# Performance work log

Measured on AMD Instinct MI355X. Metric: run time of the kernel, lower is better.

The kernel has to match this reference:

```python
import jax, jax.numpy as jnp
import numpy as np

IN_F, OUT_F, GROUP, KROT, PACK, BATCH = 4096, 14336, 128, 8, 8, 16


def _pack_nibbles(nib):
    # nib: int32 in [0,16) with shape [R, C]; pack 8 consecutive cols into one int32
    shifts = 4 * jnp.arange(PACK, dtype=jnp.int32)
    return jnp.sum(nib.reshape(nib.shape[0], -1, PACK) << shifts, axis=-1).astype(jnp.int32)


def setup_inputs() -> dict:
    key = jax.random.key(0)
    ks = jax.random.split(key, 7)
    n_groups = IN_F // GROUP
    x = jax.random.normal(ks[0], (BATCH, IN_F), dtype=jnp.float16)
    theta = (0.1 * jax.random.normal(ks[1], (KROT, IN_F // 2), dtype=jnp.float32)).astype(jnp.float16)
    # each rotation round pairs channels via a permutation: (pairs[k,2i], pairs[k,2i+1])
    pairs = jnp.stack([
        jax.random.permutation(jax.random.fold_in(ks[2], k), IN_F)
        for k in range(KROT)
    ]).astype(jnp.int32)
    channel_scales = (1.0 + 0.01 * jax.random.normal(ks[3], (1, IN_F), dtype=jnp.float32)).astype(jnp.float16)
    qweight = _pack_nibbles(jax.random.randint(ks[4], (IN_F, OUT_F), 0, 16, dtype=jnp.int32))
    qzeros = _pack_nibbles(jax.random.randint(ks[5], (n_groups, OUT_F), 0, 16, dtype=jnp.int32))
    scales = (0.001 + 0.01 * jax.random.uniform(ks[6], (n_groups, OUT_F), dtype=jnp.float32)).astype(jnp.float16)
    return {"x": x, "theta": theta, "pairs": pairs, "channel_scales": channel_scales,
            "qweight": qweight, "qzeros": qzeros, "scales": scales}


def _rotate(x, theta, pairs, channel_scales):
    # KROT rounds of pairwise Givens rotations, then per-channel scaling
    cos = jnp.cos(theta.astype(jnp.float32)).astype(x.dtype)  # [KROT, IN/2]
    sin = jnp.sin(theta.astype(jnp.float32)).astype(x.dtype)
    for k in range(theta.shape[0]):
        ia, ib = pairs[k, 0::2], pairs[k, 1::2]
        a, b = x[..., ia], x[..., ib]
        x = x.at[..., ia].set(cos[k] * a - sin[k] * b).at[..., ib].set(sin[k] * a + cos[k] * b)
    return x * channel_scales


def _dequant(qweight, qzeros, scales, group_size, dtype):
    shifts = 4 * jnp.arange(PACK, dtype=jnp.int32)
    iw = ((qweight[:, :, None] >> shifts) & 0xF).reshape(qweight.shape[0], -1)  # [IN, OUT]
    iz = ((qzeros[:, :, None] >> shifts) & 0xF).reshape(qzeros.shape[0], -1)    # [n_groups, OUT]
    w = (iw - jnp.repeat(iz, group_size, axis=0)).astype(dtype)
    return w * jnp.repeat(scales, group_size, axis=0)


def reference(x, theta, pairs, channel_scales, qweight, qzeros, scales):
    group_size = x.shape[-1] // qzeros.shape[0]
    xr = _rotate(x, theta, pairs, channel_scales)
    w = _dequant(qweight, qzeros, scales, group_size, xr.dtype)  # [IN, OUT] fp16
    return xr @ w  # [BATCH, OUT]
```

## Files before the change

kernel.cpp:

```cpp
#include <hip/hip_runtime.h>
#include <cstdint>

#define IN_F   4096
#define OUT_F  14336
#define GROUP  128
#define KROT   8
#define BATCH  16
#define NJP    1792
#define NG     32

typedef __attribute__((ext_vector_type(8))) short short8;
typedef __attribute__((ext_vector_type(4))) float f32x4;

__device__ uint32_t g_xa[BATCH * IN_F / 2];
__device__ float    g_rs[NG * BATCH];
__device__ float    g_part[4 * BATCH * OUT_F];

static __device__ __forceinline__ unsigned short f2bf(float f) {
    union { float f; uint32_t i; } v; v.f = f;
    uint32_t u = v.i;
    uint32_t r = u + 0x7FFFu + ((u >> 16) & 1u);
    return (unsigned short)(r >> 16);
}
static __device__ __forceinline__ float bf2f(uint32_t u16) {
    union { uint32_t i; float f; } v; v.i = u16 << 16; return v.f;
}

__global__ __launch_bounds__(1024) void k_rotate(
    const float* __restrict__ x,
    const float* __restrict__ theta,
    const int*   __restrict__ pairs,
    const float* __restrict__ cscale)
{
    __shared__ float row[IN_F];
    const int b   = blockIdx.x;
    const int tid = threadIdx.x;

    int2  ij0[KROT], ij1[KROT];
    float c0[KROT], s0[KROT], c1[KROT], s1[KROT];
#pragma unroll
    for (int k = 0; k < KROT; ++k) {
        const int2*  pk = (const int2*)(pairs + k * IN_F);
        const float* tk = theta + k * (IN_F / 2);
        ij0[k] = pk[tid];
        ij1[k] = pk[tid + 1024];
        __sincosf(tk[tid],        &s0[k], &c0[k]);
        __sincosf(tk[tid + 1024], &s1[k], &c1[k]);
    }

    for (int i = tid; i < IN_F; i += 1024) row[i] = x[b * IN_F + i];
    __syncthreads();

#pragma unroll
    for (int k = 0; k < KROT; ++k) {
        float a0 = row[ij0[k].x], b0 = row[ij0[k].y];
        float a1 = row[ij1[k].x], b1 = row[ij1[k].y];
        row[ij0[k].x] = c0[k] * a0 - s0[k] * b0;
        row[ij0[k].y] = s0[k] * a0 + c0[k] * b0;
        row[ij1[k].x] = c1[k] * a1 - s1[k] * b1;
        row[ij1[k].y] = s1[k] * a1 + c1[k] * b1;
        __syncthreads();
    }

    float p0, p1;
    {
        int i = tid;
        uint32_t lo = f2bf(row[2 * i]     * cscale[2 * i]);
        uint32_t hi = f2bf(row[2 * i + 1] * cscale[2 * i + 1]);
        g_xa[b * (IN_F / 2) + i] = lo | (hi << 16);
        p0 = bf2f(lo) + bf2f(hi);
        i = tid + 1024;
        lo = f2bf(row[2 * i]     * cscale[2 * i]);
        hi = f2bf(row[2 * i + 1] * cscale[2 * i + 1]);
        g_xa[b * (IN_F / 2) + i] = lo | (hi << 16);
        p1 = bf2f(lo) + bf2f(hi);
    }
#pragma unroll
    for (int m = 1; m < 64; m <<= 1) {
        p0 += __shfl_xor(p0, m, 64);
        p1 += __shfl_xor(p1, m, 64);
    }
    if ((tid & 63) == 0) {
        const int w = tid >> 6;
        g_rs[w * BATCH + b]        = p0;
        g_rs[(16 + w) * BATCH + b] = p1;
    }
}

__global__ __launch_bounds__(256) void k_gemm(
    const int*   __restrict__ qweight,
    const int*   __restrict__ qzeros,
    const float* __restrict__ scales)
{
    __shared__ uint4 ldsb[128 * 17];

    const int tid   = threadIdx.x;
    const int bn    = blockIdx.x % 112;
    const int bk    = blockIdx.x / 112;
    const int n0    = bn * 128;
    const int jp0   = n0 >> 3;
    const int jp    = tid & 15;
    const int koct  = tid >> 4;
    const int lane  = tid & 63;
    const int wv    = tid >> 6;
    const int mrow  = lane & 15;
    const int quad  = lane >> 4;
    const int xsw   = koct ^ (jp & 7);

    const int nl0 = wv * 32 + mrow;
    const int nl1 = nl0 + 16;
    const int sw0 = (nl0 >> 3) & 7;
    const int sw1 = (nl1 >> 3) & 7;

    float s0v[8], s1v[8], zf0[8], zf1[8];
    f32x4 rsv[8];
    {
        const int jz0 = jp0 + (nl0 >> 3);
        const int jz1 = jp0 + (nl1 >> 3);
        const int sh  = 4 * (mrow & 7);
#pragma unroll
        for (int g = 0; g < 8; ++g) {
            const int gg = bk * 8 + g;
            s0v[g] = scales[(size_t)gg * OUT_F + n0 + nl0];
            s1v[g] = scales[(size_t)gg * OUT_F + n0 + nl1];
            zf0[g] = 128.0f + (float)(((uint32_t)qzeros[gg * NJP + jz0] >> sh) & 15u);
            zf1[g] = 128.0f + (float)(((uint32_t)qzeros[gg * NJP + jz1] >> sh) & 15u);
            rsv[g] = *(const f32x4*)(g_rs + gg * BATCH + quad * 4);
        }
    }

    f32x4 m0 = {0.f, 0.f, 0.f, 0.f};
    f32x4 m1 = {0.f, 0.f, 0.f, 0.f};

    for (int st = 0; st < 8; ++st) {
        const int g   = bk * 8 + st;
        const int kr0 = g * GROUP + koct * 8;

        uint32_t wc[8];
#pragma unroll
        for (int i = 0; i < 8; ++i)
            wc[i] = (uint32_t)qweight[(size_t)(kr0 + i) * NJP + jp0 + jp];

        uint4 ac[4];
        const uint32_t* apst = g_xa + mrow * (IN_F / 2) + bk * 512 + st * 64 + quad * 4;
#pragma unroll
        for (int kt = 0; kt < 4; ++kt) ac[kt] = *(const uint4*)(apst + kt * 16);

#pragma unroll
        for (int c = 0; c < 8; ++c) {
            uint4 cell;
            uint32_t pk[4];
#pragma unroll
            for (int h = 0; h < 4; ++h) {
                uint32_t lo = (wc[2 * h]     >> (4 * c)) & 15u;
                uint32_t hi = (wc[2 * h + 1] >> (4 * c)) & 15u;
                pk[h] = 0x43004300u | lo | (hi << 16);
            }
            cell.x = pk[0]; cell.y = pk[1]; cell.z = pk[2]; cell.w = pk[3];
            ldsb[(jp * 8 + c) * 17 + xsw] = cell;
        }
        __syncthreads();

        f32x4 ga = {0.f, 0.f, 0.f, 0.f};
        f32x4 gb = {0.f, 0.f, 0.f, 0.f};
#pragma unroll
        for (int kt = 0; kt < 4; ++kt) {
            union { uint4 q; short8 s; } af, b0, b1;
            af.q = ac[kt];
            const int ko = kt * 4 + quad;
            b0.q = ldsb[nl0 * 17 + (ko ^ sw0)];
            b1.q = ldsb[nl1 * 17 + (ko ^ sw1)];
            ga = __builtin_amdgcn_mfma_f32_16x16x32_bf16(af.s, b0.s, ga, 0, 0, 0);
            gb = __builtin_amdgcn_mfma_f32_16x16x32_bf16(af.s, b1.s, gb, 0, 0, 0);
        }

        const float t0 = s0v[st] * zf0[st];
        const float t1 = s1v[st] * zf1[st];
#pragma unroll
        for (int r = 0; r < 4; ++r) {
            m0[r] = fmaf(s0v[st], ga[r], fmaf(-t0, rsv[st][r], m0[r]));
            m1[r] = fmaf(s1v[st], gb[r], fmaf(-t1, rsv[st][r], m1[r]));
        }
        __syncthreads();
    }

    float* pp = g_part + (size_t)bk * BATCH * OUT_F;
#pragma unroll
    for (int r = 0; r < 4; ++r) {
        const int row = quad * 4 + r;
        pp[(size_t)row * OUT_F + n0 + nl0] = m0[r];
        pp[(size_t)row * OUT_F + n0 + nl1] = m1[r];
    }
}

__global__ __launch_bounds__(128) void k_reduce(float* __restrict__ out)
{
    const int t = blockIdx.x * 128 + threadIdx.x;
    const size_t j = (size_t)t * 4;
    float4 a = *(const float4*)(g_part + j);
    float4 b = *(const float4*)(g_part + (size_t)BATCH * OUT_F + j);
    float4 c = *(const float4*)(g_part + (size_t)2 * BATCH * OUT_F + j);
    float4 d = *(const float4*)(g_part + (size_t)3 * BATCH * OUT_F + j);
    float4 s;
    s.x = (a.x + b.x) + (c.x + d.x);
    s.y = (a.y + b.y) + (c.y + d.y);
    s.z = (a.z + b.z) + (c.z + d.z);
    s.w = (a.w + b.w) + (c.w + d.w);
    *(float4*)(out + j) = s;
}

extern "C" void kernel_launch(void* const* d_in, const int* in_sizes, int n_in,
                              void* d_out, int out_size, void* d_ws, size_t ws_size,
                              hipStream_t stream) {
    const float* x       = (const float*)d_in[0];
    const float* theta   = (const float*)d_in[1];
    const int*   pairs   = (const int*)d_in[2];
    const float* cscale  = (const float*)d_in[3];
    const int*   qweight = (const int*)d_in[4];
    const int*   qzeros  = (const int*)d_in[5];
    const float* scales  = (const float*)d_in[6];
    float*       out     = (float*)d_out;
    (void)d_ws; (void)ws_size;

    k_rotate<<<16, 1024, 0, stream>>>(x, theta, pairs, cscale);
    k_gemm<<<448, 256, 0, stream>>>(qweight, qzeros, scales);
    k_reduce<<<(BATCH * OUT_F) / (128 * 4), 128, 0, stream>>>(out);
}
```

Measured before the change: 107.6 us.

## Fuse split-K reduction into GEMM via per-wave K split and LDS reduce

Each block now covers 32 output columns with its four waves splitting K, and sums the partials in LDS before writing the output directly. This removes the global partial buffer, the separate reduce kernel launch, and the block-wide barriers in the K loop, since each wave uses a private LDS region. In exchange, global weight loads become narrower per row (16-byte segments), which may reduce coalescing efficiency.

```diff
diff --git a/kernel.cpp b/kernel.cpp
--- a/kernel.cpp
+++ b/kernel.cpp
@@ -14,7 +14,6 @@
 
 __device__ uint32_t g_xa[BATCH * IN_F / 2];
 __device__ float    g_rs[NG * BATCH];
-__device__ float    g_part[4 * BATCH * OUT_F];
 
 static __device__ __forceinline__ unsigned short f2bf(float f) {
     union { float f; uint32_t i; } v; v.f = f;
@@ -90,29 +89,30 @@
 __global__ __launch_bounds__(256) void k_gemm(
     const int*   __restrict__ qweight,
     const int*   __restrict__ qzeros,
-    const float* __restrict__ scales)
+    const float* __restrict__ scales,
+    float*       __restrict__ out)
 {
-    __shared__ uint4 ldsb[128 * 17];
-
-    const int tid   = threadIdx.x;
-    const int bn    = blockIdx.x % 112;
-    const int bk    = blockIdx.x / 112;
-    const int n0    = bn * 128;
-    const int jp0   = n0 >> 3;
-    const int jp    = tid & 15;
-    const int koct  = tid >> 4;
-    const int lane  = tid & 63;
-    const int wv    = tid >> 6;
-    const int mrow  = lane & 15;
-    const int quad  = lane >> 4;
-    const int xsw   = koct ^ (jp & 7);
-
-    const int nl0 = wv * 32 + mrow;
-    const int nl1 = nl0 + 16;
-    const int sw0 = (nl0 >> 3) & 7;
-    const int sw1 = (nl1 >> 3) & 7;
-
-    float s0v[8], s1v[8], zf0[8], zf1[8];
+    __shared__ uint4 ldsb[4 * 32 * 17];
+
+    const int tid  = threadIdx.x;
+    const int bn   = blockIdx.x;
+    const int n0   = bn * 32;
+    const int jp0  = bn * 4;
+    const int w    = tid >> 6;
+    const int lane = tid & 63;
+    const int jps  = lane & 3;
+    const int koct = lane >> 2;
+    const int mrow = lane & 15;
+    const int quad = lane >> 4;
+    const int nl0  = mrow;
+    const int nl1  = mrow + 16;
+    const int sw0  = mrow >> 3;
+    const int sw1  = 2 + (mrow >> 3);
+    const int xsw  = koct ^ jps;
+
+    uint4* ldsw = ldsb + w * (32 * 17);
+
+    float s0v[8], s1v[8], t0v[8], t1v[8];
     f32x4 rsv[8];
     {
         const int jz0 = jp0 + (nl0 >> 3);
@@ -120,11 +120,13 @@
         const int sh  = 4 * (mrow & 7);
 #pragma unroll
         for (int g = 0; g < 8; ++g) {
-            const int gg = bk * 8 + g;
+            const int gg = w * 8 + g;
             s0v[g] = scales[(size_t)gg * OUT_F + n0 + nl0];
             s1v[g] = scales[(size_t)gg * OUT_F + n0 + nl1];
-            zf0[g] = 128.0f + (float)(((uint32_t)qzeros[gg * NJP + jz0] >> sh) & 15u);
-            zf1[g] = 128.0f + (float)(((uint32_t)qzeros[gg * NJP + jz1] >> sh) & 15u);
+            const float z0 = 128.0f + (float)(((uint32_t)qzeros[gg * NJP + jz0] >> sh) & 15u);
+            const float z1 = 128.0f + (float)(((uint32_t)qzeros[gg * NJP + jz1] >> sh) & 15u);
+            t0v[g] = s0v[g] * z0;
+            t1v[g] = s1v[g] * z1;
             rsv[g] = *(const f32x4*)(g_rs + gg * BATCH + quad * 4);
         }
     }
@@ -133,16 +135,16 @@
     f32x4 m1 = {0.f, 0.f, 0.f, 0.f};
 
     for (int st = 0; st < 8; ++st) {
-        const int g   = bk * 8 + st;
+        const int g   = w * 8 + st;
         const int kr0 = g * GROUP + koct * 8;
 
         uint32_t wc[8];
 #pragma unroll
         for (int i = 0; i < 8; ++i)
-            wc[i] = (uint32_t)qweight[(size_t)(kr0 + i) * NJP + jp0 + jp];
+            wc[i] = (uint32_t)qweight[(size_t)(kr0 + i) * NJP + jp0 + jps];
 
         uint4 ac[4];
-        const uint32_t* apst = g_xa + mrow * (IN_F / 2) + bk * 512 + st * 64 + quad * 4;
+        const uint32_t* apst = g_xa + mrow * (IN_F / 2) + w * 512 + st * 64 + quad * 4;
 #pragma unroll
         for (int kt = 0; kt < 4; ++kt) ac[kt] = *(const uint4*)(apst + kt * 16);
 
@@ -157,9 +159,8 @@
                 pk[h] = 0x43004300u | lo | (hi << 16);
             }
             cell.x = pk[0]; cell.y = pk[1]; cell.z = pk[2]; cell.w = pk[3];
-            ldsb[(jp * 8 + c) * 17 + xsw] = cell;
-        }
-        __syncthreads();
+            ldsw[(jps * 8 + c) * 17 + xsw] = cell;
+        }
 
         f32x4 ga = {0.f, 0.f, 0.f, 0.f};
         f32x4 gb = {0.f, 0.f, 0.f, 0.f};
@@ -168,45 +169,41 @@
             union { uint4 q; short8 s; } af, b0, b1;
             af.q = ac[kt];
             const int ko = kt * 4 + quad;
-            b0.q = ldsb[nl0 * 17 + (ko ^ sw0)];
-            b1.q = ldsb[nl1 * 17 + (ko ^ sw1)];
+            b0.q = ldsw[nl0 * 17 + (ko ^ sw0)];
+            b1.q = ldsw[nl1 * 17 + (ko ^ sw1)];
             ga = __builtin_amdgcn_mfma_f32_16x16x32_bf16(af.s, b0.s, ga, 0, 0, 0);
             gb = __builtin_amdgcn_mfma_f32_16x16x32_bf16(af.s, b1.s, gb, 0, 0, 0);
         }
 
-        const float t0 = s0v[st] * zf0[st];
-        const float t1 = s1v[st] * zf1[st];
 #pragma unroll
         for (int r = 0; r < 4; ++r) {
-            m0[r] = fmaf(s0v[st], ga[r], fmaf(-t0, rsv[st][r], m0[r]));
-            m1[r] = fmaf(s1v[st], gb[r], fmaf(-t1, rsv[st][r], m1[r]));
-        }
-        __syncthreads();
-    }
-
-    float* pp = g_part + (size_t)bk * BATCH * OUT_F;
+            m0[r] = fmaf(s0v[st], ga[r], fmaf(-t0v[st], rsv[st][r], m0[r]));
+            m1[r] = fmaf(s1v[st], gb[r], fmaf(-t1v[st], rsv[st][r], m1[r]));
+        }
+    }
+
+    float* redw = (float*)(ldsb + w * (32 * 17));
 #pragma unroll
     for (int r = 0; r < 4; ++r) {
-        const int row = quad * 4 + r;
-        pp[(size_t)row * OUT_F + n0 + nl0] = m0[r];
-        pp[(size_t)row * OUT_F + n0 + nl1] = m1[r];
-    }
-}
-
-__global__ __launch_bounds__(128) void k_reduce(float* __restrict__ out)
-{
-    const int t = blockIdx.x * 128 + threadIdx.x;
-    const size_t j = (size_t)t * 4;
-    float4 a = *(const float4*)(g_part + j);
-    float4 b = *(const float4*)(g_part + (size_t)BATCH * OUT_F + j);
-    float4 c = *(const float4*)(g_part + (size_t)2 * BATCH * OUT_F + j);
-    float4 d = *(const float4*)(g_part + (size_t)3 * BATCH * OUT_F + j);
-    float4 s;
-    s.x = (a.x + b.x) + (c.x + d.x);
-    s.y = (a.y + b.y) + (c.y + d.y);
-    s.z = (a.z + b.z) + (c.z + d.z);
-    s.w = (a.w + b.w) + (c.w + d.w);
-    *(float4*)(out + j) = s;
+        redw[(quad * 4 + r) * 16 + mrow]       = m0[r];
+        redw[256 + (quad * 4 + r) * 16 + mrow] = m1[r];
+    }
+    __syncthreads();
+
+    const float* redf = (const float*)ldsb;
+    const int col  = tid & 31;
+    const int tile = col >> 4;
+    const int c16  = col & 15;
+    const int r0   = tid >> 5;
+    float sA = 0.f, sB = 0.f;
+#pragma unroll
+    for (int ww = 0; ww < 4; ++ww) {
+        const float* base = redf + ww * (32 * 17 * 4) + tile * 256 + c16;
+        sA += base[r0 * 16];
+        sB += base[(r0 + 8) * 16];
+    }
+    out[(size_t)r0 * OUT_F + n0 + col]       = sA;
+    out[(size_t)(r0 + 8) * OUT_F + n0 + col] = sB;
 }
 
 extern "C" void kernel_launch(void* const* d_in, const int* in_sizes, int n_in,
@@ -223,6 +220,5 @@
     (void)d_ws; (void)ws_size;
 
     k_rotate<<<16, 1024, 0, stream>>>(x, theta, pairs, cscale);
-    k_gemm<<<448, 256, 0, stream>>>(qweight, qzeros, scales);
-    k_reduce<<<(BATCH * OUT_F) / (128 * 4), 128, 0, stream>>>(out);
-}
+    k_gemm<<<448, 256, 0, stream>>>(qweight, qzeros, scales, out);
+}
```

Result: slower. 127.3 us (+18.3%).

## Split K across waves in gemm, removing per-stage block barriers

Applied to the files above, without the earlier changes.

Reworks the dequant GEMM so that each wave owns two quantization groups and all 128 output columns, instead of the whole block sharing each K stage. Each wave dequantizes into its own LDS region, so the two __syncthreads per stage disappear. The four waves' partial results are then reduced through LDS once at the end and written with vectorized stores. This trades more registers per thread (8 accumulators, per-group scale tables) and an extra LDS reduction for less barrier stalling and better coalesced output. Occupancy is hinted through launch_bounds(256,2).

```diff
diff --git a/kernel.cpp b/kernel.cpp
--- a/kernel.cpp
+++ b/kernel.cpp
@@ -87,110 +87,124 @@
     }
 }
 
-__global__ __launch_bounds__(256) void k_gemm(
+__global__ __launch_bounds__(256, 2) void k_gemm(
     const int*   __restrict__ qweight,
     const int*   __restrict__ qzeros,
     const float* __restrict__ scales)
 {
-    __shared__ uint4 ldsb[128 * 17];
-
-    const int tid   = threadIdx.x;
-    const int bn    = blockIdx.x % 112;
-    const int bk    = blockIdx.x / 112;
-    const int n0    = bn * 128;
-    const int jp0   = n0 >> 3;
-    const int jp    = tid & 15;
-    const int koct  = tid >> 4;
-    const int lane  = tid & 63;
-    const int wv    = tid >> 6;
-    const int mrow  = lane & 15;
-    const int quad  = lane >> 4;
-    const int xsw   = koct ^ (jp & 7);
-
-    const int nl0 = wv * 32 + mrow;
-    const int nl1 = nl0 + 16;
-    const int sw0 = (nl0 >> 3) & 7;
-    const int sw1 = (nl1 >> 3) & 7;
-
-    float s0v[8], s1v[8], zf0[8], zf1[8];
-    f32x4 rsv[8];
+    __shared__ uint4 ldsb[4 * 512];
+
+    const int tid  = threadIdx.x;
+    const int bn   = blockIdx.x % 112;
+    const int bk   = blockIdx.x / 112;
+    const int n0   = bn * 128;
+    const int jp0  = bn * 16;
+    const int w    = tid >> 6;
+    const int lane = tid & 63;
+    const int jp   = lane & 15;
+    const int rr   = lane >> 4;
+    const int mrow = lane & 15;
+    const int quad = lane >> 4;
+
+    uint4* ldsw = ldsb + w * 512;
+
+    float sv[2][8], tv[2][8];
+    f32x4 rsv[2];
     {
-        const int jz0 = jp0 + (nl0 >> 3);
-        const int jz1 = jp0 + (nl1 >> 3);
-        const int sh  = 4 * (mrow & 7);
-#pragma unroll
-        for (int g = 0; g < 8; ++g) {
-            const int gg = bk * 8 + g;
-            s0v[g] = scales[(size_t)gg * OUT_F + n0 + nl0];
-            s1v[g] = scales[(size_t)gg * OUT_F + n0 + nl1];
-            zf0[g] = 128.0f + (float)(((uint32_t)qzeros[gg * NJP + jz0] >> sh) & 15u);
-            zf1[g] = 128.0f + (float)(((uint32_t)qzeros[gg * NJP + jz1] >> sh) & 15u);
-            rsv[g] = *(const f32x4*)(g_rs + gg * BATCH + quad * 4);
+        const int sh = 4 * (mrow & 7);
+#pragma unroll
+        for (int gi = 0; gi < 2; ++gi) {
+            const int gg = bk * 8 + w * 2 + gi;
+            rsv[gi] = *(const f32x4*)(g_rs + gg * BATCH + quad * 4);
+#pragma unroll
+            for (int t = 0; t < 8; ++t) {
+                const int col = n0 + t * 16 + mrow;
+                const float s = scales[(size_t)gg * OUT_F + col];
+                const float z = 128.0f +
+                    (float)(((uint32_t)qzeros[gg * NJP + (col >> 3)] >> sh) & 15u);
+                sv[gi][t] = s;
+                tv[gi][t] = s * z;
+            }
         }
     }
 
-    f32x4 m0 = {0.f, 0.f, 0.f, 0.f};
-    f32x4 m1 = {0.f, 0.f, 0.f, 0.f};
-
-    for (int st = 0; st < 8; ++st) {
-        const int g   = bk * 8 + st;
-        const int kr0 = g * GROUP + koct * 8;
-
-        uint32_t wc[8];
-#pragma unroll
-        for (int i = 0; i < 8; ++i)
-            wc[i] = (uint32_t)qweight[(size_t)(kr0 + i) * NJP + jp0 + jp];
-
-        uint4 ac[4];
-        const uint32_t* apst = g_xa + mrow * (IN_F / 2) + bk * 512 + st * 64 + quad * 4;
-#pragma unroll
-        for (int kt = 0; kt < 4; ++kt) ac[kt] = *(const uint4*)(apst + kt * 16);
-
-#pragma unroll
-        for (int c = 0; c < 8; ++c) {
-            uint4 cell;
-            uint32_t pk[4];
-#pragma unroll
-            for (int h = 0; h < 4; ++h) {
-                uint32_t lo = (wc[2 * h]     >> (4 * c)) & 15u;
-                uint32_t hi = (wc[2 * h + 1] >> (4 * c)) & 15u;
-                pk[h] = 0x43004300u | lo | (hi << 16);
+    f32x4 m[8];
+#pragma unroll
+    for (int t = 0; t < 8; ++t) m[t] = (f32x4){0.f, 0.f, 0.f, 0.f};
+
+#pragma unroll
+    for (int gi = 0; gi < 2; ++gi) {
+        const int gg = bk * 8 + w * 2 + gi;
+
+        f32x4 ga[8];
+#pragma unroll
+        for (int t = 0; t < 8; ++t) ga[t] = (f32x4){0.f, 0.f, 0.f, 0.f};
+
+#pragma unroll
+        for (int sc = 0; sc < 4; ++sc) {
+            const int kr0 = gg * GROUP + sc * 32 + rr * 8;
+
+            uint32_t wc[8];
+#pragma unroll
+            for (int i = 0; i < 8; ++i)
+                wc[i] = (uint32_t)qweight[(size_t)(kr0 + i) * NJP + jp0 + jp];
+
+            union { uint4 q; short8 s; } af;
+            af.q = *(const uint4*)(g_xa + mrow * (IN_F / 2)
+                                   + ((gg * GROUP + sc * 32) >> 1) + quad * 4);
+
+#pragma unroll
+            for (int cc = 0; cc < 8; ++cc) {
+                const int c  = cc ^ (jp & 7);
+                const int sh = 4 * c;
+                uint4 cell;
+                uint32_t pk[4];
+#pragma unroll
+                for (int h = 0; h < 4; ++h) {
+                    uint32_t lo = (wc[2 * h]     >> sh) & 15u;
+                    uint32_t hi = (wc[2 * h + 1] >> sh) & 15u;
+                    pk[h] = 0x43004300u | lo | (hi << 16);
+                }
+                cell.x = pk[0]; cell.y = pk[1]; cell.z = pk[2]; cell.w = pk[3];
+                ldsw[rr * 128 + jp * 8 + c] = cell;
             }
-            cell.x = pk[0]; cell.y = pk[1]; cell.z = pk[2]; cell.w = pk[3];
-            ldsb[(jp * 8 + c) * 17 + xsw] = cell;
+
+#pragma unroll
+            for (int t = 0; t < 8; ++t) {
+                union { uint4 q; short8 s; } bf;
+                bf.q = ldsw[quad * 128 + t * 16 + mrow];
+                ga[t] = __builtin_amdgcn_mfma_f32_16x16x32_bf16(af.s, bf.s, ga[t], 0, 0, 0);
+            }
         }
-        __syncthreads();
-
-        f32x4 ga = {0.f, 0.f, 0.f, 0.f};
-        f32x4 gb = {0.f, 0.f, 0.f, 0.f};
-#pragma unroll
-        for (int kt = 0; kt < 4; ++kt) {
-            union { uint4 q; short8 s; } af, b0, b1;
-            af.q = ac[kt];
-            const int ko = kt * 4 + quad;
-            b0.q = ldsb[nl0 * 17 + (ko ^ sw0)];
-            b1.q = ldsb[nl1 * 17 + (ko ^ sw1)];
-            ga = __builtin_amdgcn_mfma_f32_16x16x32_bf16(af.s, b0.s, ga, 0, 0, 0);
-            gb = __builtin_amdgcn_mfma_f32_16x16x32_bf16(af.s, b1.s, gb, 0, 0, 0);
-        }
-
-        const float t0 = s0v[st] * zf0[st];
-        const float t1 = s1v[st] * zf1[st];
-#pragma unroll
-        for (int r = 0; r < 4; ++r) {
-            m0[r] = fmaf(s0v[st], ga[r], fmaf(-t0, rsv[st][r], m0[r]));
-            m1[r] = fmaf(s1v[st], gb[r], fmaf(-t1, rsv[st][r], m1[r]));
-        }
-        __syncthreads();
-    }
-
-    float* pp = g_part + (size_t)bk * BATCH * OUT_F;
-#pragma unroll
-    for (int r = 0; r < 4; ++r) {
-        const int row = quad * 4 + r;
-        pp[(size_t)row * OUT_F + n0 + nl0] = m0[r];
-        pp[(size_t)row * OUT_F + n0 + nl1] = m1[r];
-    }
+
+#pragma unroll
+        for (int t = 0; t < 8; ++t)
+#pragma unroll
+            for (int r = 0; r < 4; ++r)
+                m[t][r] = fmaf(sv[gi][t], ga[t][r],
+                               fmaf(-tv[gi][t], rsv[gi][r], m[t][r]));
+    }
+
+    float* fw = (float*)ldsb + w * 2048;
+#pragma unroll
+    for (int t = 0; t < 8; ++t)
+#pragma unroll
+        for (int r = 0; r < 4; ++r)
+            fw[(quad * 4 + r) * 128 + t * 16 + mrow] = m[t][r];
+    __syncthreads();
+
+    const float* fb   = (const float*)ldsb;
+    const int    colg = (tid & 31) * 4;
+    const int    row  = tid >> 5;
+    f32x4 sA = {0.f, 0.f, 0.f, 0.f}, sB = {0.f, 0.f, 0.f, 0.f};
+#pragma unroll
+    for (int ww = 0; ww < 4; ++ww) {
+        sA += *(const f32x4*)(fb + ww * 2048 + row * 128 + colg);
+        sB += *(const f32x4*)(fb + ww * 2048 + (row + 8) * 128 + colg);
+    }
+    float* pp = g_part + (size_t)bk * BATCH * OUT_F + n0 + colg;
+    *(f32x4*)(pp + (size_t)row * OUT_F)       = sA;
+    *(f32x4*)(pp + (size_t)(row + 8) * OUT_F) = sB;
 }
 
 __global__ __launch_bounds__(128) void k_reduce(float* __restrict__ out)
```

Measured after the change: 102.6 us. -4.6%, faster.
